# Optimization experiments

Hardware: AMD Instinct MI355X
Metric: run time of the kernel (lower is better)

## Reference

```python
import jax, jax.numpy as jnp
import numpy as np

CH, XH, YH, RADIUS = 2, 2, 2, 1  # channel_heads, x_heads, y_heads, neighborhood radius


def neighborhood_mask(n_sub_x, n_sub_y, radius):
    # clamped neighbor offsets reduce to |di|<=r and |dj|<=r within the grid
    iy = jnp.arange(n_sub_y)
    ix = jnp.arange(n_sub_x)
    my = jnp.abs(iy[:, None] - iy[None, :]) <= radius  # [ny, ny]
    mx = jnp.abs(ix[:, None] - ix[None, :]) <= radius  # [nx, nx]
    m = my[:, None, :, None] & mx[None, :, None, :]    # [ny, nx, ny, nx]
    s = n_sub_x * n_sub_y
    return m.reshape(s, s)  # row-major (h1 w1)(h2 w2), matching einops


def setup_inputs() -> dict:
    key = jax.random.key(0)
    k1, k2, k3 = jax.random.split(key, 3)
    C = 128
    seq = jax.random.normal(k1, (2, 256, C, 16, 16), dtype=jnp.float32)
    w_qkv = jax.random.normal(k2, (3 * C, C), dtype=jnp.float32) / np.sqrt(C).astype(np.float32)
    w_out = jax.random.normal(k3, (C, C), dtype=jnp.float32) / np.sqrt(C).astype(np.float32)
    b_out = jnp.zeros((C,), dtype=jnp.float32)
    return {"seq": seq, "w_qkv": w_qkv, "w_out": w_out, "b_out": b_out,
            "n_sub_x": 16, "n_sub_y": 16}


def reference(seq, w_qkv, w_out, b_out, n_sub_x, n_sub_y):
    b, s, C, H, W = seq.shape
    h, w = H // YH, W // XH
    c = C // CH
    nH = YH * XH * CH  # total heads

    # pointwise qkv projection over channels: [b, s, 3C, H, W]
    qkv = jnp.einsum('bschw,dc->bsdhw', seq, w_qkv)

    # decompose2d: split spatial grid into y_heads x x_heads blocks -> spatial heads
    # [b, s, 3C, YH, h, XH, w] -> [b, s, YH*XH, 3C, h, w]
    qkv = qkv.reshape(b, s, 3 * C, YH, h, XH, w)
    qkv = qkv.transpose(0, 1, 3, 5, 2, 4, 6).reshape(b, s, YH * XH, 3 * C, h, w)

    # split into q,k,v and channel heads: 3C = 3 * CH * c
    qkv = qkv.reshape(b, s, YH * XH, 3, CH, c, h, w)
    # -> [3, b, (spatial_heads * channel_heads), s, c, h, w]
    qkv = qkv.transpose(3, 0, 2, 4, 1, 5, 6, 7).reshape(3, b, nH, s, c, h, w)
    q, k, v = qkv[0], qkv[1], qkv[2]

    # scaled dot-product attention over flattened function dim (c,h,w)
    scale = 1.0 / np.sqrt(c * h * w).astype(np.float32)
    scores = jnp.einsum('bnschw,bntchw->bnst', q, k) * scale  # [b, nH, s, s]
    mask = neighborhood_mask(n_sub_x, n_sub_y, RADIUS)  # [s, s]
    scores = jnp.where(mask[None, None, :, :], scores, jnp.finfo(scores.dtype).min)
    attn = jax.nn.softmax(scores, axis=-1)
    sa = jnp.einsum('bnst,bntchw->bnschw', attn, v)  # [b, nH, s, c, h, w]

    # merge channel heads back: [b, s, spatial_heads, C, h, w]
    sa = sa.reshape(b, YH * XH, CH, s, c, h, w)
    sa = sa.transpose(0, 3, 1, 2, 4, 5, 6).reshape(b, s, YH, XH, C, h, w)
    # recompose2d: [b, s, C, H, W]
    sa = sa.transpose(0, 1, 4, 2, 5, 3, 6).reshape(b, s, C, H, W)

    # output pointwise projection with bias
    out = jnp.einsum('bschw,dc->bsdhw', sa, w_out) + b_out[None, None, :, None, None]
    return out
```

## Files before the change

### kernel.cpp

```cpp
#include <hip/hip_runtime.h>

#define BATCH 2
#define SS    256
#define CC    128
#define HWN   256
#define FDIM  4096

typedef unsigned int uint;
typedef unsigned short ushort;
typedef short bf16x8 __attribute__((ext_vector_type(8)));
typedef ushort us4 __attribute__((ext_vector_type(4)));
typedef float f32x4 __attribute__((ext_vector_type(4)));

__device__ __forceinline__ ushort f2b(float f) {
  uint u = __float_as_uint(f);
  return (ushort)((u + 0x7fffu + ((u >> 16) & 1u)) >> 16);
}
__device__ __forceinline__ float b2f(ushort h) { return __uint_as_float((uint)h << 16); }

__global__ void k_convert(const float* __restrict__ wqkv, const float* __restrict__ wout,
                          ushort* __restrict__ wqkv_b, ushort* __restrict__ wout_b) {
  int i = blockIdx.x * 256 + threadIdx.x;
  if (i < 384 * 128) wqkv_b[i] = f2b(wqkv[i]);
  if (i < 128 * 128) {
    const int cc = i & 127;
    const int ks = cc >> 5, qq = (cc >> 3) & 3, j = cc & 7;
    const int creal = (ks >> 1) * 64 + ((((ks & 1) << 1) | (qq >> 1)) << 4)
                      + ((qq & 1) << 3) + j;
    wout_b[i] = f2b(wout[(i >> 7) * 128 + creal]);
  }
}

__global__ __launch_bounds__(256) void k_qkv(const float* __restrict__ seq,
                                             const ushort* __restrict__ wqkv_b,
                                             ushort* __restrict__ qkvh) {
  __shared__ ushort wlds[128 * 128];
  const int blk = blockIdx.x;
  const int qkvi = blk >> 9, bs = blk & 511;
  const int b = bs >> 8, s = bs & 255;
  const int t = threadIdx.x;
  const int wave = t >> 6, lane = t & 63;
  const int qq = lane >> 4, m = lane & 15;

  const float* sp = seq + (size_t)bs * (CC * HWN);

  bf16x8 bfrag[4][4];
  #pragma unroll
  for (int ntp = 0; ntp < 4; ++ntp) {
    const int hw = (wave * 4 + ntp) * 16 + m;
    #pragma unroll
    for (int ks = 0; ks < 4; ++ks) {
      const int k0 = ks * 32 + qq * 8;
      float tmp[8];
      #pragma unroll
      for (int j = 0; j < 8; ++j) tmp[j] = sp[(k0 + j) * HWN + hw];
      bf16x8 fr;
      #pragma unroll
      for (int j = 0; j < 8; ++j) fr[j] = (short)f2b(tmp[j]);
      bfrag[ntp][ks] = fr;
    }
  }

  #pragma unroll
  for (int i = 0; i < 8; ++i) {
    const int row = i * 16 + (t >> 4), col16 = t & 15;
    bf16x8 w = *(const bf16x8*)(wqkv_b + (qkvi * 128 + row) * 128 + col16 * 8);
    *(bf16x8*)&wlds[row * 128 + ((col16 ^ (row & 15)) * 8)] = w;
  }
  __syncthreads();

  #pragma unroll
  for (int mt8 = 0; mt8 < 8; ++mt8) {
    bf16x8 afrag[4];
    #pragma unroll
    for (int ks = 0; ks < 4; ++ks)
      afrag[ks] = *(const bf16x8*)&wlds[(mt8 * 16 + m) * 128 + (((ks * 4 + qq) ^ m) * 8)];
    const int ch = mt8 >> 2, m4 = mt8 & 3;
    #pragma unroll
    for (int ntp = 0; ntp < 4; ++ntp) {
      f32x4 acc = {0.f, 0.f, 0.f, 0.f};
      #pragma unroll
      for (int ks = 0; ks < 4; ++ks)
        acc = __builtin_amdgcn_mfma_f32_16x16x32_bf16(afrag[ks], bfrag[ntp][ks], acc, 0, 0, 0);
      const int ntg = wave * 4 + ntp;
      const int n   = ((ntg >> 3) * 2 + (m >> 3)) * 2 + ch;
      const int hwl = (ntg & 7) * 8 + (m & 7);
      const size_t base = ((size_t)(qkvi * 16 + b * 8 + n) * SS + s) * FDIM;
      us4 pk;
      #pragma unroll
      for (int r = 0; r < 4; ++r) pk[r] = f2b(acc[r]);
      *(us4*)(qkvh + base + m4 * 1024 + hwl * 16 + qq * 4) = pk;
    }
  }
}

__global__ __launch_bounds__(1024) void k_scores(const ushort* __restrict__ qkvh,
                                                 float* __restrict__ attn) {
  __shared__ float red[16][64][12];
  const int unit = blockIdx.x;
  const int b  = unit >> 7;
  const int n  = (unit >> 4) & 7;
  const int sy = unit & 15;
  const int t = threadIdx.x;
  const int wave = t >> 6, lane = t & 63;
  const int qq = lane >> 4, l15 = lane & 15;
  const size_t hs = (size_t)SS * FDIM;
  const ushort* qb = qkvh + (size_t)(b * 8 + n) * hs;
  const ushort* kb = qkvh + (size_t)(16 + b * 8 + n) * hs;

  const ushort* qp = qb + (size_t)(sy * 16 + l15) * FDIM + qq * 8;
  const ushort* kp[3];
  #pragma unroll
  for (int tl = 0; tl < 3; ++tl) {
    const int tyc = min(max(sy - 1 + tl, 0), 15);
    kp[tl] = kb + (size_t)(tyc * 16 + l15) * FDIM + qq * 8;
  }

  f32x4 acc[3] = {{0,0,0,0},{0,0,0,0},{0,0,0,0}};
  const int kbeg = wave * 256;
  #pragma unroll
  for (int it = 0; it < 4; ++it) {
    const int k0 = kbeg + it * 64;
    bf16x8 a0 = *(const bf16x8*)(qp + k0);
    bf16x8 a1 = *(const bf16x8*)(qp + k0 + 32);
    bf16x8 b0[3], b1[3];
    #pragma unroll
    for (int tl = 0; tl < 3; ++tl) {
      b0[tl] = *(const bf16x8*)(kp[tl] + k0);
      b1[tl] = *(const bf16x8*)(kp[tl] + k0 + 32);
    }
    #pragma unroll
    for (int tl = 0; tl < 3; ++tl)
      acc[tl] = __builtin_amdgcn_mfma_f32_16x16x32_bf16(a0, b0[tl], acc[tl], 0, 0, 0);
    #pragma unroll
    for (int tl = 0; tl < 3; ++tl)
      acc[tl] = __builtin_amdgcn_mfma_f32_16x16x32_bf16(a1, b1[tl], acc[tl], 0, 0, 0);
  }

  #pragma unroll
  for (int tl = 0; tl < 3; ++tl)
    #pragma unroll
    for (int r = 0; r < 4; ++r) red[wave][lane][tl * 4 + r] = acc[tl][r];
  __syncthreads();
  if (t < 768) {
    const int lane2 = t / 12, idx = t - lane2 * 12;
    float ssum = red[0][lane2][idx];
    #pragma unroll
    for (int w = 1; w < 16; ++w) ssum += red[w][lane2][idx];
    red[0][lane2][idx] = ssum;
  }
  __syncthreads();
  if (wave != 0) return;
  #pragma unroll
  for (int tl = 0; tl < 3; ++tl)
    #pragma unroll
    for (int r = 0; r < 4; ++r) acc[tl][r] = red[0][lane][tl * 4 + r];

  const int tx = l15;
  float sc[3][4];
  #pragma unroll
  for (int tl = 0; tl < 3; ++tl) {
    const int ty = sy - 1 + tl;
    const bool tyv = (ty >= 0 && ty < 16);
    #pragma unroll
    for (int r = 0; r < 4; ++r) {
      const int sx = qq * 4 + r;
      const bool v = tyv && (tx - sx <= 1) && (sx - tx <= 1);
      sc[tl][r] = v ? acc[tl][r] * (1.f / 64.f) : -1e30f;
    }
  }
  #pragma unroll
  for (int r = 0; r < 4; ++r) {
    float mx = fmaxf(fmaxf(sc[0][r], sc[1][r]), sc[2][r]);
    #pragma unroll
    for (int off = 1; off < 16; off <<= 1) mx = fmaxf(mx, __shfl_xor(mx, off));
    float p[3], sum = 0.f;
    #pragma unroll
    for (int tl = 0; tl < 3; ++tl) { p[tl] = __expf(sc[tl][r] - mx); sum += p[tl]; }
    #pragma unroll
    for (int off = 1; off < 16; off <<= 1) sum += __shfl_xor(sum, off);
    const float inv = 1.f / sum;
    const int sx = qq * 4 + r;
    const int s = sy * 16 + sx;
    #pragma unroll
    for (int tl = 0; tl < 3; ++tl) {
      const int ty = sy - 1 + tl;
      const int dxp = tx - sx + 1;
      if (ty >= 0 && ty < 16 && dxp >= 0 && dxp <= 2)
        attn[((size_t)(b * 8 + n) * SS + s) * 9 + tl * 3 + dxp] = p[tl] * inv;
    }
  }
}

__global__ __launch_bounds__(256) void k_out(const ushort* __restrict__ qkvh,
                                             const float* __restrict__ attn,
                                             const ushort* __restrict__ wout_b,
                                             const float* __restrict__ bout,
                                             float* __restrict__ out) {
  __shared__ ushort wlds[128 * 128];
  const int blk = blockIdx.x;
  const int bs = blk >> 2, sub = blk & 3;
  const int b = bs >> 8, s = bs & 255;
  const int t = threadIdx.x;
  const int wave = t >> 6, lane = t & 63;
  const int ntg = sub * 4 + wave;
  const int qq = lane >> 4, m = lane & 15;
  const int sy = s >> 4, sx = s & 15;
  const size_t hs = (size_t)SS * FDIM;

  #pragma unroll
  for (int i = 0; i < 8; ++i) {
    const int row = i * 16 + (t >> 4), col16 = t & 15;
    bf16x8 w = *(const bf16x8*)(wout_b + row * 128 + col16 * 8);
    *(bf16x8*)&wlds[row * 128 + ((col16 ^ (row & 15)) * 8)] = w;
  }

  int sjc[9];
  bool vld[9];
  #pragma unroll
  for (int j = 0; j < 9; ++j) {
    const int ny = sy + j / 3 - 1, nx = sx + j % 3 - 1;
    vld[j] = (ny >= 0 && ny < 16 && nx >= 0 && nx < 16);
    sjc[j] = min(max(ny, 0), 15) * 16 + min(max(nx, 0), 15);
  }

  const int nbase = ((ntg >> 3) * 2 + (m >> 3)) * 2;
  float pch[2][9];
  #pragma unroll
  for (int ch = 0; ch < 2; ++ch) {
    #pragma unroll
    for (int j = 0; j < 9; ++j) {
      const float w = attn[((size_t)(b * 8 + nbase + ch) * SS + s) * 9 + j];
      pch[ch][j] = vld[j] ? w : 0.f;
    }
  }

  const int hwl = (ntg & 7) * 8 + (m & 7);
  bf16x8 bfrag[4];
  #pragma unroll
  for (int ks = 0; ks < 4; ++ks) {
    const int ch = ks >> 1;
    const int c64hi = ((ks & 1) << 1) | (qq >> 1);
    const int half = qq & 1;
    const ushort* vb = qkvh + (size_t)(32 + b * 8 + nbase + ch) * hs;
    const int off = c64hi * 1024 + hwl * 16 + half * 8;
    float facc[8] = {0.f, 0.f, 0.f, 0.f, 0.f, 0.f, 0.f, 0.f};
    #pragma unroll
    for (int j = 0; j < 9; ++j) {
      bf16x8 vv = *(const bf16x8*)(vb + (size_t)sjc[j] * FDIM + off);
      const float pj = pch[ch][j];
      #pragma unroll
      for (int e = 0; e < 8; ++e) facc[e] += pj * b2f((ushort)vv[e]);
    }
    bf16x8 fr;
    #pragma unroll
    for (int e = 0; e < 8; ++e) fr[e] = (short)f2b(facc[e]);
    bfrag[ks] = fr;
  }

  __syncthreads();

  #pragma unroll
  for (int mt = 0; mt < 8; ++mt) {
    bf16x8 afrag[4];
    #pragma unroll
    for (int ks = 0; ks < 4; ++ks)
      afrag[ks] = *(const bf16x8*)&wlds[(mt * 16 + m) * 128 + (((ks * 4 + qq) ^ m) * 8)];
    f32x4 acc = {0.f, 0.f, 0.f, 0.f};
    #pragma unroll
    for (int ks = 0; ks < 4; ++ks)
      acc = __builtin_amdgcn_mfma_f32_16x16x32_bf16(afrag[ks], bfrag[ks], acc, 0, 0, 0);
    const int hw = ntg * 16 + m;
    #pragma unroll
    for (int r = 0; r < 4; ++r) {
      const int d = mt * 16 + qq * 4 + r;
      out[((size_t)bs * CC + d) * HWN + hw] = acc[r] + bout[d];
    }
  }
}

extern "C" void kernel_launch(void* const* d_in, const int* in_sizes, int n_in,
                              void* d_out, int out_size, void* d_ws, size_t ws_size,
                              hipStream_t stream) {
  const float* seq  = (const float*)d_in[0];
  const float* wqkv = (const float*)d_in[1];
  const float* wout = (const float*)d_in[2];
  const float* bout = (const float*)d_in[3];
  char* ws = (char*)d_ws;
  ushort* wqkv_b = (ushort*)(ws);
  ushort* wout_b = (ushort*)(ws + 98304);
  ushort* qkvh   = (ushort*)(ws + 131072);
  float*  attn   = (float*)(ws + 131072 + 100663296ull);
  float*  outp   = (float*)d_out;

  hipLaunchKernelGGL(k_convert, dim3(192),  dim3(256), 0, stream, wqkv, wout, wqkv_b, wout_b);
  hipLaunchKernelGGL(k_qkv,     dim3(1536), dim3(256), 0, stream, seq, wqkv_b, qkvh);
  hipLaunchKernelGGL(k_scores,  dim3(256),  dim3(1024), 0, stream, qkvh, attn);
  hipLaunchKernelGGL(k_out,     dim3(2048), dim3(256), 0, stream, qkvh, attn, wout_b, bout, outp);
}
```

Before: 212.9 us.

## Load seq once per block for q/k/v; remap blocks for XCD locality

```diff
diff --git a/kernel.cpp b/kernel.cpp
--- a/kernel.cpp
+++ b/kernel.cpp
@@ -36,55 +36,54 @@
                                              ushort* __restrict__ qkvh) {
   __shared__ ushort wlds[128 * 128];
   const int blk = blockIdx.x;
-  const int qkvi = blk >> 9, bs = blk & 511;
+  const int bs = blk >> 2, hq = blk & 3;
   const int b = bs >> 8, s = bs & 255;
   const int t = threadIdx.x;
   const int wave = t >> 6, lane = t & 63;
   const int qq = lane >> 4, m = lane & 15;
+  const int ntg = hq * 4 + wave;
+  const int hw = ntg * 16 + m;
 
   const float* sp = seq + (size_t)bs * (CC * HWN);
 
-  bf16x8 bfrag[4][4];
-  #pragma unroll
-  for (int ntp = 0; ntp < 4; ++ntp) {
-    const int hw = (wave * 4 + ntp) * 16 + m;
-    #pragma unroll
-    for (int ks = 0; ks < 4; ++ks) {
-      const int k0 = ks * 32 + qq * 8;
-      float tmp[8];
+  bf16x8 bfrag[4];
+  #pragma unroll
+  for (int ks = 0; ks < 4; ++ks) {
+    const int k0 = ks * 32 + qq * 8;
+    float tmp[8];
+    #pragma unroll
+    for (int j = 0; j < 8; ++j) tmp[j] = sp[(k0 + j) * HWN + hw];
+    bf16x8 fr;
+    #pragma unroll
+    for (int j = 0; j < 8; ++j) fr[j] = (short)f2b(tmp[j]);
+    bfrag[ks] = fr;
+  }
+
+  const int n_qk = ((ntg >> 3) * 2 + (m >> 3)) * 2;
+  const int hwl  = (ntg & 7) * 8 + (m & 7);
+
+  for (int qkvi = 0; qkvi < 3; ++qkvi) {
+    if (qkvi > 0) __syncthreads();
+    #pragma unroll
+    for (int i = 0; i < 8; ++i) {
+      const int row = i * 16 + (t >> 4), col16 = t & 15;
+      bf16x8 w = *(const bf16x8*)(wqkv_b + (qkvi * 128 + row) * 128 + col16 * 8);
+      *(bf16x8*)&wlds[row * 128 + ((col16 ^ (row & 15)) * 8)] = w;
+    }
+    __syncthreads();
+
+    #pragma unroll
+    for (int mt8 = 0; mt8 < 8; ++mt8) {
+      bf16x8 afrag[4];
       #pragma unroll
-      for (int j = 0; j < 8; ++j) tmp[j] = sp[(k0 + j) * HWN + hw];
-      bf16x8 fr;
-      #pragma unroll
-      for (int j = 0; j < 8; ++j) fr[j] = (short)f2b(tmp[j]);
-      bfrag[ntp][ks] = fr;
-    }
-  }
-
-  #pragma unroll
-  for (int i = 0; i < 8; ++i) {
-    const int row = i * 16 + (t >> 4), col16 = t & 15;
-    bf16x8 w = *(const bf16x8*)(wqkv_b + (qkvi * 128 + row) * 128 + col16 * 8);
-    *(bf16x8*)&wlds[row * 128 + ((col16 ^ (row & 15)) * 8)] = w;
-  }
-  __syncthreads();
-
-  #pragma unroll
-  for (int mt8 = 0; mt8 < 8; ++mt8) {
-    bf16x8 afrag[4];
-    #pragma unroll
-    for (int ks = 0; ks < 4; ++ks)
-      afrag[ks] = *(const bf16x8*)&wlds[(mt8 * 16 + m) * 128 + (((ks * 4 + qq) ^ m) * 8)];
-    const int ch = mt8 >> 2, m4 = mt8 & 3;
-    #pragma unroll
-    for (int ntp = 0; ntp < 4; ++ntp) {
+      for (int ks = 0; ks < 4; ++ks)
+        afrag[ks] = *(const bf16x8*)&wlds[(mt8 * 16 + m) * 128 + (((ks * 4 + qq) ^ m) * 8)];
+      const int ch = mt8 >> 2, m4 = mt8 & 3;
       f32x4 acc = {0.f, 0.f, 0.f, 0.f};
       #pragma unroll
       for (int ks = 0; ks < 4; ++ks)
-        acc = __builtin_amdgcn_mfma_f32_16x16x32_bf16(afrag[ks], bfrag[ntp][ks], acc, 0, 0, 0);
-      const int ntg = wave * 4 + ntp;
-      const int n   = ((ntg >> 3) * 2 + (m >> 3)) * 2 + ch;
-      const int hwl = (ntg & 7) * 8 + (m & 7);
+        acc = __builtin_amdgcn_mfma_f32_16x16x32_bf16(afrag[ks], bfrag[ks], acc, 0, 0, 0);
+      const int n = n_qk + ch;
       const size_t base = ((size_t)(qkvi * 16 + b * 8 + n) * SS + s) * FDIM;
       us4 pk;
       #pragma unroll
@@ -97,7 +96,8 @@
 __global__ __launch_bounds__(1024) void k_scores(const ushort* __restrict__ qkvh,
                                                  float* __restrict__ attn) {
   __shared__ float red[16][64][12];
-  const int unit = blockIdx.x;
+  const int g = blockIdx.x;
+  const int unit = (g & 7) * 32 + (g >> 3);
   const int b  = unit >> 7;
   const int n  = (unit >> 4) & 7;
   const int sy = unit & 15;
@@ -198,14 +198,18 @@
                                              const float* __restrict__ bout,
                                              float* __restrict__ out) {
   __shared__ ushort wlds[128 * 128];
-  const int blk = blockIdx.x;
-  const int bs = blk >> 2, sub = blk & 3;
-  const int b = bs >> 8, s = bs & 255;
+  const int g = blockIdx.x;
+  const int r9 = g >> 3;
+  const int G = (g & 7) * 4 + (r9 >> 6);
+  const int idx = r9 & 63;
+  const int b = G >> 4, sy = G & 15;
+  const int sx = idx >> 2, sub = idx & 3;
+  const int s = sy * 16 + sx;
+  const int bs = b * 256 + s;
   const int t = threadIdx.x;
   const int wave = t >> 6, lane = t & 63;
   const int ntg = sub * 4 + wave;
   const int qq = lane >> 4, m = lane & 15;
-  const int sy = s >> 4, sx = s & 15;
   const size_t hs = (size_t)SS * FDIM;
 
   #pragma unroll
@@ -294,7 +298,7 @@
   float*  outp   = (float*)d_out;
 
   hipLaunchKernelGGL(k_convert, dim3(192),  dim3(256), 0, stream, wqkv, wout, wqkv_b, wout_b);
-  hipLaunchKernelGGL(k_qkv,     dim3(1536), dim3(256), 0, stream, seq, wqkv_b, qkvh);
+  hipLaunchKernelGGL(k_qkv,     dim3(2048), dim3(256), 0, stream, seq, wqkv_b, qkvh);
   hipLaunchKernelGGL(k_scores,  dim3(256),  dim3(1024), 0, stream, qkvh, attn);
   hipLaunchKernelGGL(k_out,     dim3(2048), dim3(256), 0, stream, qkvh, attn, wout_b, bout, outp);
 }
```

After: 190.0 us. 1.12x faster.
